# Kernel tuning notes

Measured on AMD Instinct MI355X. Metric: run time of the kernel, lower is better.

The kernel has to match this reference:

```python
import jax, jax.numpy as jnp
import numpy as np

N_NODES = 50000
N_EDGES = 800000
N_FEAT = 100
N_CLASSES = 40
K_HOPS = 2


def setup_inputs() -> dict:
    key = jax.random.key(0)
    k1, k2, k3, k4 = jax.random.split(key, 4)
    x = jax.random.normal(k1, (N_NODES, N_FEAT), dtype=jnp.float32)
    edge_index = jax.random.randint(k2, (2, N_EDGES), 0, N_NODES, dtype=jnp.int64)
    # linear layer params (PyG Linear: x @ W^T + b); store W as [F, C] for x @ W
    W = jax.random.normal(k3, (N_FEAT, N_CLASSES), dtype=jnp.float32) / np.sqrt(N_FEAT)
    b = jax.random.normal(k4, (N_CLASSES,), dtype=jnp.float32) * 0.01
    return {"x": x, "edge_index": edge_index, "W": W, "b": b}


def _gcn_norm(edge_index, num_nodes):
    # add self-loops with weight 1, compute symmetric normalization D^-1/2 A D^-1/2
    loop = jnp.arange(num_nodes, dtype=edge_index.dtype)
    row = jnp.concatenate([edge_index[0], loop])  # source
    col = jnp.concatenate([edge_index[1], loop])  # target
    w = jnp.ones(row.shape[0], dtype=jnp.float32)
    deg = jax.ops.segment_sum(w, col, num_segments=num_nodes)
    dinv = jnp.where(deg > 0, jax.lax.rsqrt(jnp.maximum(deg, 1.0)), 0.0)
    norm = dinv[row] * dinv[col]  # [E + N]
    return row, col, norm


def reference(x, edge_index, W, b):
    n = x.shape[0]
    row, col, norm = _gcn_norm(edge_index, n)
    # K-hop propagation: gather at source, scale, scatter-add at target
    h = x
    for _ in range(K_HOPS):
        msg = norm[:, None] * h[row]          # [E+N, F] edge-wise gather + scale
        h = jax.ops.segment_sum(msg, col, num_segments=n)  # scatter-add
    logits = h @ W + b                        # [N, C]
    return jax.nn.log_softmax(logits, axis=1)
```

## Files before the change

### kernel.cpp

```cpp
#include <hip/hip_runtime.h>
#include <hip/hip_fp16.h>
#include <hip/hip_fp8.h>
#include <math.h>

#define N_NODES 50000
#define N_EDGES 800000
#define N_FEAT 100
#define N_CLASSES 40
#define ROWB 64
#define N_SLICES 8
#define SLICE_NODES 6250
#define N_CHUNKS 125
#define EPC 6400
#define CF_BLOCKS (N_SLICES * N_CHUNKS)
#define SCAN_BLK 256
#define N_SCAN_BLKS 196
#define CONV_UNITS 3125
#define LIN_UNITS 1954
#define N_SUPER 391
#define CL_BLOCKS (N_SUPER * 13)

typedef unsigned int nt_uint4 __attribute__((ext_vector_type(4)));


__device__ __forceinline__ unsigned char f2q(float x) {
    __hip_fp8_e4m3 q(x);
    return (unsigned char)q.__x;
}
__device__ __forceinline__ float q2f(unsigned char b) {
    __hip_fp8_e4m3 q;
    q.__x = (__hip_fp8_storage_t)b;
    return (float)q;
}


__global__ void k_conv_lin(const void* __restrict__ ei,
                           unsigned int* __restrict__ epack,
                           const float* __restrict__ x, const float* __restrict__ W,
                           unsigned char* __restrict__ y0q) {
    __shared__ float4 Ws[N_CLASSES / 4][N_FEAT + 1];
    int super = blockIdx.x / 13;
    int pos = blockIdx.x - super * 13;
    if (pos < 8) {
        int unit = super * 8 + pos;
        if (unit >= CONV_UNITS) return;
        int e = unit * 256 + threadIdx.x;
        long long v = __builtin_nontemporal_load((const long long*)ei + e);
        bool bad = (v < 0 || v >= N_NODES);
        bool is32 = (__ballot(bad) != 0ull);
        unsigned int r, c;
        if (is32) {
            const unsigned int* p = (const unsigned int*)ei;
            r = __builtin_nontemporal_load(p + e);
            c = __builtin_nontemporal_load(p + N_EDGES + e);
        } else {
            r = (unsigned int)v;
            c = (unsigned int)__builtin_nontemporal_load((const long long*)ei + N_EDGES + e);
        }
        epack[e] = r | (c << 16);
    } else {
        int unit = super * 5 + (pos - 8);
        if (unit >= LIN_UNITS) return;
        for (int i = threadIdx.x; i < N_FEAT * (N_CLASSES / 4); i += blockDim.x) {
            int k = i / (N_CLASSES / 4), c4 = i - k * (N_CLASSES / 4);
            Ws[c4][k] = ((const float4*)W)[i];
        }
        __syncthreads();
        int idx = unit * 256 + threadIdx.x;
        if (idx >= N_NODES * (N_CLASSES / 4)) return;
        int n = idx / (N_CLASSES / 4);
        int c4 = idx - n * (N_CLASSES / 4);
        const float* hr = x + (size_t)n * N_FEAT;
        float4 s = {0.f, 0.f, 0.f, 0.f};
#pragma unroll
        for (int k = 0; k < N_FEAT; ++k) {
            float hv = hr[k];
            float4 w = Ws[c4][k];
            s.x += hv * w.x; s.y += hv * w.y; s.z += hv * w.z; s.w += hv * w.w;
        }
        uchar4 q = make_uchar4(f2q(s.x), f2q(s.y), f2q(s.z), f2q(s.w));
        *(uchar4*)(y0q + (size_t)n * ROWB + c4 * 4) = q;
    }
}


__global__ void k_count(const unsigned int* __restrict__ epack, int* __restrict__ dp) {
    __shared__ int hist[SLICE_NODES];
    int slice = blockIdx.x & (N_SLICES - 1);
    int chunk = blockIdx.x >> 3;
    unsigned int lo = slice * SLICE_NODES;
    for (int i = threadIdx.x; i < SLICE_NODES; i += blockDim.x) hist[i] = 0;
    __syncthreads();
    int g0 = chunk * (EPC / 4), g1 = g0 + (EPC / 4);
    for (int g = g0 + threadIdx.x; g < g1; g += blockDim.x) {
        uint4 p4 = ((const uint4*)epack)[g];
        unsigned int c0 = p4.x >> 16, c1 = p4.y >> 16, c2 = p4.z >> 16, c3 = p4.w >> 16;
        if (c0 - lo < SLICE_NODES) atomicAdd(&hist[c0 - lo], 1);
        if (c1 - lo < SLICE_NODES) atomicAdd(&hist[c1 - lo], 1);
        if (c2 - lo < SLICE_NODES) atomicAdd(&hist[c2 - lo], 1);
        if (c3 - lo < SLICE_NODES) atomicAdd(&hist[c3 - lo], 1);
    }
    __syncthreads();
    int* dpk = dp + (size_t)chunk * N_NODES + lo;
    for (int i = threadIdx.x; i < SLICE_NODES; i += blockDim.x) dpk[i] = hist[i];
}


__global__ void k_scan1(int* __restrict__ dp, int* __restrict__ offs,
                        int* __restrict__ sums, float* __restrict__ dinv,
                        unsigned short* __restrict__ dinv16) {
    __shared__ int s[SCAN_BLK];
    int i = blockIdx.x * SCAN_BLK + threadIdx.x;
    int run = 0;
    if (i < N_NODES) {
#pragma unroll 5
        for (int k = 0; k < N_CHUNKS; ++k) {
            int* p = dp + (size_t)k * N_NODES + i;
            int t = *p;
            *p = run;
            run += t;
        }
        float d = rsqrtf((float)run + 1.0f);
        dinv[i] = d;
        dinv16[i] = __half_as_ushort(__float2half_rn(d));
    }
    s[threadIdx.x] = (i < N_NODES) ? run : 0;
    __syncthreads();
    int v = s[threadIdx.x];
    for (int off = 1; off < SCAN_BLK; off <<= 1) {
        int t = (threadIdx.x >= off) ? s[threadIdx.x - off] : 0;
        __syncthreads();
        s[threadIdx.x] += t;
        __syncthreads();
    }
    if (i < N_NODES) offs[i] = s[threadIdx.x] - v;
    if (threadIdx.x == SCAN_BLK - 1) sums[blockIdx.x] = s[SCAN_BLK - 1];
}

__global__ void k_scan3(int* __restrict__ offs, const int* __restrict__ sums,
                        unsigned int* __restrict__ csr) {
    __shared__ int sc[SCAN_BLK];
    __shared__ int orig[SCAN_BLK];
    int t = threadIdx.x;
    int v = (t < N_SCAN_BLKS) ? sums[t] : 0;
    sc[t] = v; orig[t] = v;
    __syncthreads();
    for (int off = 1; off < SCAN_BLK; off <<= 1) {
        int u = (t >= off) ? sc[t - off] : 0;
        __syncthreads();
        sc[t] += u;
        __syncthreads();
    }
    int base = sc[blockIdx.x] - orig[blockIdx.x];
    int i = blockIdx.x * SCAN_BLK + t;
    if (i < N_NODES) offs[i] += base;
    if (i == 0) offs[N_NODES] = N_EDGES;
    if (blockIdx.x == 0 && t < 16) csr[N_EDGES + t] = 0u;
}


__global__ void k_fill(const unsigned int* __restrict__ epack,
                       const unsigned short* __restrict__ dinv16,
                       const int* __restrict__ offs, const int* __restrict__ dp,
                       unsigned int* __restrict__ csr) {
    __shared__ int pos[SLICE_NODES];
    int slice = blockIdx.x & (N_SLICES - 1);
    int chunk = blockIdx.x >> 3;
    unsigned int lo = slice * SLICE_NODES;
    const int* dpk = dp + (size_t)chunk * N_NODES + lo;
    const int* ofs = offs + lo;
    for (int i = threadIdx.x; i < SLICE_NODES; i += blockDim.x)
        pos[i] = ofs[i] + dpk[i];
    __syncthreads();
    int g0 = chunk * (EPC / 4), g1 = g0 + (EPC / 4);
    for (int g = g0 + threadIdx.x; g < g1; g += blockDim.x) {
        uint4 p4 = ((const uint4*)epack)[g];
#pragma unroll
        for (int j = 0; j < 4; ++j) {
            unsigned int p = (j == 0) ? p4.x : (j == 1) ? p4.y : (j == 2) ? p4.z : p4.w;
            unsigned int c = p >> 16;
            if (c - lo < SLICE_NODES) {
                unsigned int r = p & 0xffffu;
                int pp = atomicAdd(&pos[c - lo], 1);
                csr[pp] = r | ((unsigned int)dinv16[r] << 16);
            }
        }
    }
}


#define GPROC(Q, K, ACC)                                                         \
    {                                                                            \
        unsigned int q_ = (Q);                                                   \
        int idx_ = base + (K);                                                   \
        bool in_ = (idx_ >= s && idx_ < e);                                      \
        unsigned int r_ = in_ ? (q_ & 0xffffu) : 0u;                             \
        float vv_ = q2f(sl[(size_t)r_ * ROWB]);                                  \
        unsigned int wb_ = in_ ? (q_ >> 16) : 0u;                                \
        ACC += __half2float(__ushort_as_half((unsigned short)wb_)) * vv_;        \
    }

template <bool LSM, typename DstT, int DSTRIDE>
__global__ void k_gather(const int* __restrict__ offs, const unsigned int* __restrict__ csr,
                         const unsigned char* __restrict__ src, const float* __restrict__ dinv,
                         DstT* __restrict__ dst, const float* __restrict__ bias) {
    int wave = threadIdx.x >> 6;
    int lane = threadIdx.x & 63;
    int n = blockIdx.x * 4 + wave;
    if (n >= N_NODES) return;
    int s = offs[n], e = offs[n + 1];
    bool act = (lane < N_CLASSES);
    float dc = dinv[n];
    const unsigned char* sl = src + lane;
    float acc0 = 0.0f, acc1 = 0.0f, acc2 = 0.0f, acc3 = 0.0f;
    if (act) acc0 = dc * q2f(sl[(size_t)n * ROWB]);
    for (int base = (s & ~15); base < e; base += 16) {
        nt_uint4 q0 = __builtin_nontemporal_load((const nt_uint4*)(csr + base));
        nt_uint4 q1 = __builtin_nontemporal_load((const nt_uint4*)(csr + base + 4));
        nt_uint4 q2 = __builtin_nontemporal_load((const nt_uint4*)(csr + base + 8));
        nt_uint4 q3 = __builtin_nontemporal_load((const nt_uint4*)(csr + base + 12));
        if (act) {
            GPROC(q0[0],  0, acc0) GPROC(q0[1],  1, acc1) GPROC(q0[2],  2, acc2) GPROC(q0[3],  3, acc3)
            GPROC(q1[0],  4, acc0) GPROC(q1[1],  5, acc1) GPROC(q1[2],  6, acc2) GPROC(q1[3],  7, acc3)
            GPROC(q2[0],  8, acc0) GPROC(q2[1],  9, acc1) GPROC(q2[2], 10, acc2) GPROC(q2[3], 11, acc3)
            GPROC(q3[0], 12, acc0) GPROC(q3[1], 13, acc1) GPROC(q3[2], 14, acc2) GPROC(q3[3], 15, acc3)
        }
    }
    float acc = dc * ((acc0 + acc1) + (acc2 + acc3));
    if (!LSM) {
        if (act) {
            if constexpr (sizeof(DstT) == 1)
                dst[(size_t)n * DSTRIDE + lane] = (DstT)f2q(acc);
            else
                dst[(size_t)n * DSTRIDE + lane] = (DstT)acc;
        }
    } else {
        float v = act ? acc + bias[lane] : -INFINITY;
        float m = v;
#pragma unroll
        for (int off = 32; off; off >>= 1) m = fmaxf(m, __shfl_xor(m, off));
        float ex = act ? __expf(v - m) : 0.0f;
        float ssum = ex;
#pragma unroll
        for (int off = 32; off; off >>= 1) ssum += __shfl_xor(ssum, off);
        float ls = logf(ssum);
        if (act) dst[(size_t)n * DSTRIDE + lane] = (DstT)(v - m - ls);
    }
}


extern "C" void kernel_launch(void* const* d_in, const int* in_sizes, int n_in,
                              void* d_out, int out_size, void* d_ws, size_t ws_size,
                              hipStream_t stream) {
    const float* x = (const float*)d_in[0];
    const void* ei = d_in[1];
    const float* W = (const float*)d_in[2];
    const float* b = (const float*)d_in[3];
    float* z = (float*)d_out;

    char* ws = (char*)d_ws;
    size_t o = 0;
    auto alloc = [&](size_t bytes) { char* p = ws + o; o += (bytes + 255) & ~(size_t)255; return p; };
    unsigned int*   epack  = (unsigned int*)alloc((size_t)N_EDGES * 4);
    int*            dp     = (int*)alloc((size_t)N_CHUNKS * N_NODES * 4);
    float*          dinv   = (float*)alloc(N_NODES * 4);
    unsigned short* dinv16 = (unsigned short*)alloc(N_NODES * 2);
    int*            offs   = (int*)alloc((N_NODES + 1) * 4);
    int*            sums   = (int*)alloc(SCAN_BLK * 4);
    unsigned int*   csr    = (unsigned int*)alloc((size_t)(N_EDGES + 16) * 4);
    unsigned char*  y0q    = (unsigned char*)alloc((size_t)N_NODES * ROWB);
    unsigned char*  h1q    = (unsigned char*)alloc((size_t)N_NODES * ROWB);

    const int T = 256;

    k_conv_lin<<<CL_BLOCKS, T, 0, stream>>>(ei, epack, x, W, y0q);

    k_count<<<CF_BLOCKS, T, 0, stream>>>(epack, dp);

    k_scan1<<<N_SCAN_BLKS, SCAN_BLK, 0, stream>>>(dp, offs, sums, dinv, dinv16);
    k_scan3<<<N_SCAN_BLKS, SCAN_BLK, 0, stream>>>(offs, sums, csr);

    k_fill<<<CF_BLOCKS, T, 0, stream>>>(epack, dinv16, offs, dp, csr);

    k_gather<false, unsigned char, ROWB><<<N_NODES / 4, T, 0, stream>>>(offs, csr, y0q, dinv, h1q, b);
    k_gather<true, float, N_CLASSES><<<N_NODES / 4, T, 0, stream>>>(offs, csr, h1q, dinv, z, b);
}
```

Measured before the change: 137.7 us.

## Pad CSR rows to multiples of eight and drop per-edge bounds checks

Each node's CSR segment is rounded up to a multiple of 8 entries. The padding is zeroed by extra blocks added to the conversion/linear kernel, so a padded entry holds weight 0 and points at row 0. The gather loop now starts at the aligned segment start, reads 8 entries per step and skips the per-edge range test and selects. This removes the waste of scanning from a 16-aligned base, but the CSR buffer grows and extra zero-weight gathers are done for the padding. FP8 decoding also uses the hardware cvt builtin when it is available.

```diff
diff --git a/kernel.cpp b/kernel.cpp
--- a/kernel.cpp
+++ b/kernel.cpp
@@ -15,10 +15,13 @@
 #define CF_BLOCKS (N_SLICES * N_CHUNKS)
 #define SCAN_BLK 256
 #define N_SCAN_BLKS 196
+#define PAD 8
 #define CONV_UNITS 3125
 #define LIN_UNITS 1954
+#define ZERO_UNITS 1173
 #define N_SUPER 391
-#define CL_BLOCKS (N_SUPER * 13)
+#define CL_BLOCKS (N_SUPER * 16)
+#define CSR_ALLOC_ENTRIES (ZERO_UNITS * 256 * 4)
 
 typedef unsigned int nt_uint4 __attribute__((ext_vector_type(4)));
 
@@ -27,20 +30,26 @@
     __hip_fp8_e4m3 q(x);
     return (unsigned char)q.__x;
 }
-__device__ __forceinline__ float q2f(unsigned char b) {
+#if __has_builtin(__builtin_amdgcn_cvt_f32_fp8)
+__device__ __forceinline__ float q2f(unsigned int b) {
+    return __builtin_amdgcn_cvt_f32_fp8((int)b, 0);
+}
+#else
+__device__ __forceinline__ float q2f(unsigned int b) {
     __hip_fp8_e4m3 q;
-    q.__x = (__hip_fp8_storage_t)b;
+    q.__x = (__hip_fp8_storage_t)(b & 0xffu);
     return (float)q;
 }
+#endif
 
 
 __global__ void k_conv_lin(const void* __restrict__ ei,
                            unsigned int* __restrict__ epack,
                            const float* __restrict__ x, const float* __restrict__ W,
-                           unsigned char* __restrict__ y0q) {
+                           unsigned char* __restrict__ y0q, unsigned int* __restrict__ csr) {
     __shared__ float4 Ws[N_CLASSES / 4][N_FEAT + 1];
-    int super = blockIdx.x / 13;
-    int pos = blockIdx.x - super * 13;
+    int super = blockIdx.x >> 4;
+    int pos = blockIdx.x & 15;
     if (pos < 8) {
         int unit = super * 8 + pos;
         if (unit >= CONV_UNITS) return;
@@ -58,7 +67,7 @@
             c = (unsigned int)__builtin_nontemporal_load((const long long*)ei + N_EDGES + e);
         }
         epack[e] = r | (c << 16);
-    } else {
+    } else if (pos < 13) {
         int unit = super * 5 + (pos - 8);
         if (unit >= LIN_UNITS) return;
         for (int i = threadIdx.x; i < N_FEAT * (N_CLASSES / 4); i += blockDim.x) {
@@ -80,6 +89,10 @@
         }
         uchar4 q = make_uchar4(f2q(s.x), f2q(s.y), f2q(s.z), f2q(s.w));
         *(uchar4*)(y0q + (size_t)n * ROWB + c4 * 4) = q;
+    } else {
+        int unit = super * 3 + (pos - 13);
+        if (unit >= ZERO_UNITS) return;
+        ((uint4*)csr)[unit * 256 + threadIdx.x] = make_uint4(0u, 0u, 0u, 0u);
     }
 }
 
@@ -111,8 +124,9 @@
                         unsigned short* __restrict__ dinv16) {
     __shared__ int s[SCAN_BLK];
     int i = blockIdx.x * SCAN_BLK + threadIdx.x;
-    int run = 0;
+    int padded = 0;
     if (i < N_NODES) {
+        int run = 0;
 #pragma unroll 5
         for (int k = 0; k < N_CHUNKS; ++k) {
             int* p = dp + (size_t)k * N_NODES + i;
@@ -123,8 +137,9 @@
         float d = rsqrtf((float)run + 1.0f);
         dinv[i] = d;
         dinv16[i] = __half_as_ushort(__float2half_rn(d));
-    }
-    s[threadIdx.x] = (i < N_NODES) ? run : 0;
+        padded = (run + PAD - 1) & ~(PAD - 1);
+    }
+    s[threadIdx.x] = padded;
     __syncthreads();
     int v = s[threadIdx.x];
     for (int off = 1; off < SCAN_BLK; off <<= 1) {
@@ -137,8 +152,7 @@
     if (threadIdx.x == SCAN_BLK - 1) sums[blockIdx.x] = s[SCAN_BLK - 1];
 }
 
-__global__ void k_scan3(int* __restrict__ offs, const int* __restrict__ sums,
-                        unsigned int* __restrict__ csr) {
+__global__ void k_scan3(int* __restrict__ offs, const int* __restrict__ sums) {
     __shared__ int sc[SCAN_BLK];
     __shared__ int orig[SCAN_BLK];
     int t = threadIdx.x;
@@ -154,8 +168,7 @@
     int base = sc[blockIdx.x] - orig[blockIdx.x];
     int i = blockIdx.x * SCAN_BLK + t;
     if (i < N_NODES) offs[i] += base;
-    if (i == 0) offs[N_NODES] = N_EDGES;
-    if (blockIdx.x == 0 && t < 16) csr[N_EDGES + t] = 0u;
+    if (blockIdx.x == 0 && t == N_SCAN_BLKS - 1) offs[N_NODES] = sc[t];
 }
 
 
@@ -189,15 +202,11 @@
 }
 
 
-#define GPROC(Q, K, ACC)                                                         \
+#define GPROC(Q, ACC)                                                            \
     {                                                                            \
         unsigned int q_ = (Q);                                                   \
-        int idx_ = base + (K);                                                   \
-        bool in_ = (idx_ >= s && idx_ < e);                                      \
-        unsigned int r_ = in_ ? (q_ & 0xffffu) : 0u;                             \
-        float vv_ = q2f(sl[(size_t)r_ * ROWB]);                                  \
-        unsigned int wb_ = in_ ? (q_ >> 16) : 0u;                                \
-        ACC += __half2float(__ushort_as_half((unsigned short)wb_)) * vv_;        \
+        float vv_ = q2f(sl[(size_t)(q_ & 0xffffu) * ROWB]);                      \
+        ACC += __half2float(__ushort_as_half((unsigned short)(q_ >> 16))) * vv_; \
     }
 
 template <bool LSM, typename DstT, int DSTRIDE>
@@ -214,16 +223,12 @@
     const unsigned char* sl = src + lane;
     float acc0 = 0.0f, acc1 = 0.0f, acc2 = 0.0f, acc3 = 0.0f;
     if (act) acc0 = dc * q2f(sl[(size_t)n * ROWB]);
-    for (int base = (s & ~15); base < e; base += 16) {
+    for (int base = s; base < e; base += 8) {
         nt_uint4 q0 = __builtin_nontemporal_load((const nt_uint4*)(csr + base));
         nt_uint4 q1 = __builtin_nontemporal_load((const nt_uint4*)(csr + base + 4));
-        nt_uint4 q2 = __builtin_nontemporal_load((const nt_uint4*)(csr + base + 8));
-        nt_uint4 q3 = __builtin_nontemporal_load((const nt_uint4*)(csr + base + 12));
         if (act) {
-            GPROC(q0[0],  0, acc0) GPROC(q0[1],  1, acc1) GPROC(q0[2],  2, acc2) GPROC(q0[3],  3, acc3)
-            GPROC(q1[0],  4, acc0) GPROC(q1[1],  5, acc1) GPROC(q1[2],  6, acc2) GPROC(q1[3],  7, acc3)
-            GPROC(q2[0],  8, acc0) GPROC(q2[1],  9, acc1) GPROC(q2[2], 10, acc2) GPROC(q2[3], 11, acc3)
-            GPROC(q3[0], 12, acc0) GPROC(q3[1], 13, acc1) GPROC(q3[2], 14, acc2) GPROC(q3[3], 15, acc3)
+            GPROC(q0[0], acc0) GPROC(q0[1], acc1) GPROC(q0[2], acc2) GPROC(q0[3], acc3)
+            GPROC(q1[0], acc0) GPROC(q1[1], acc1) GPROC(q1[2], acc2) GPROC(q1[3], acc3)
         }
     }
     float acc = dc * ((acc0 + acc1) + (acc2 + acc3));
@@ -267,18 +272,18 @@
     unsigned short* dinv16 = (unsigned short*)alloc(N_NODES * 2);
     int*            offs   = (int*)alloc((N_NODES + 1) * 4);
     int*            sums   = (int*)alloc(SCAN_BLK * 4);
-    unsigned int*   csr    = (unsigned int*)alloc((size_t)(N_EDGES + 16) * 4);
+    unsigned int*   csr    = (unsigned int*)alloc((size_t)CSR_ALLOC_ENTRIES * 4);
     unsigned char*  y0q    = (unsigned char*)alloc((size_t)N_NODES * ROWB);
     unsigned char*  h1q    = (unsigned char*)alloc((size_t)N_NODES * ROWB);
 
     const int T = 256;
 
-    k_conv_lin<<<CL_BLOCKS, T, 0, stream>>>(ei, epack, x, W, y0q);
+    k_conv_lin<<<CL_BLOCKS, T, 0, stream>>>(ei, epack, x, W, y0q, csr);
 
     k_count<<<CF_BLOCKS, T, 0, stream>>>(epack, dp);
 
     k_scan1<<<N_SCAN_BLKS, SCAN_BLK, 0, stream>>>(dp, offs, sums, dinv, dinv16);
-    k_scan3<<<N_SCAN_BLKS, SCAN_BLK, 0, stream>>>(offs, sums, csr);
+    k_scan3<<<N_SCAN_BLKS, SCAN_BLK, 0, stream>>>(offs, sums);
 
     k_fill<<<CF_BLOCKS, T, 0, stream>>>(epack, dinv16, offs, dp, csr);
 
```

Measured after the change: 133.4 us. -3.1%, faster.
